# Kernel optimization log

Hardware: AMD Instinct MI355X
Metric: run time of the kernel (lower is better)

Reference implementation:

```python
import jax, jax.numpy as jnp
import numpy as np
from jax import lax


def get_grid(h, w):
    # normalized [-1,1] grid, channel 0 = x, channel 1 = y, shape [1,h,w,2]
    gx, gy = jnp.meshgrid(jnp.linspace(-1.0, 1.0, w), jnp.linspace(-1.0, 1.0, h))
    return jnp.stack([gx, gy], axis=-1)[None].astype(jnp.float32)


def gaussian_kernel(k, sigma=1.0):
    c = jnp.arange(k, dtype=jnp.float32) - (k - 1) / 2.0
    g = jnp.exp(-(c ** 2) / (2.0 * sigma ** 2))
    k2 = jnp.outer(g, g)
    return k2 / k2.sum()


def resize_bilinear(x, H, W):
    # x: [B,C,h,w]; torch F.interpolate(mode='bilinear', align_corners=False)
    B, C, h, w = x.shape
    def coords(n_out, n_in):
        c = (jnp.arange(n_out, dtype=jnp.float32) + 0.5) * (n_in / n_out) - 0.5
        c = jnp.clip(c, 0.0, n_in - 1.0)
        lo = jnp.floor(c).astype(jnp.int32)
        hi = jnp.minimum(lo + 1, n_in - 1)
        return lo, hi, c - lo.astype(jnp.float32)
    y0, y1, wy = coords(H, h)
    x0, x1, wx = coords(W, w)
    r = x[:, :, y0, :] * (1.0 - wy)[None, None, :, None] + x[:, :, y1, :] * wy[None, None, :, None]
    return r[:, :, :, x0] * (1.0 - wx) + r[:, :, :, x1] * wx


def _forward(src_grid, kernel, src_grid_base, tgt_grid, niter):
    B = src_grid.shape[0]
    H, W = tgt_grid.shape[1], tgt_grid.shape[2]
    ks = kernel.shape[-1]
    HW = H * W
    # forward displacement, resampled to target resolution, in pixel units
    dsrc = (src_grid - src_grid_base).transpose(0, 3, 1, 2)        # [B,2,Hs,Ws]
    dsrc = resize_bilinear(dsrc, H, W)                              # [B,2,H,W]
    dx = dsrc[:, 0].reshape(B, HW) * (W / 2.0)
    dy = dsrc[:, 1].reshape(B, HW) * (H / 2.0)
    xg = (jnp.arange(HW) % W).astype(jnp.float32)
    yg = (jnp.arange(HW) // W).astype(jnp.float32)
    xi = jnp.round(xg[None] + dx).astype(jnp.int32)
    yi = jnp.round(yg[None] + dy).astype(jnp.int32)
    oob = (xi < 0) | (yi < 0) | (xi > W - 1) | (yi > H - 1)
    field = jnp.where(oob, -1, yi * W + xi) + 1   # index 0 = trash slot
    # sort + dedup: duplicates are redirected to the trash slot
    order = jnp.argsort(field, axis=1)            # stable
    sf = jnp.take_along_axis(field, order, axis=1)
    keep = jnp.concatenate([jnp.ones((B, 1), bool), sf[:, 1:] != sf[:, :-1]], axis=1)
    sf = sf * keep
    inv_order = jnp.argsort(order, axis=1)
    field = jnp.take_along_axis(sf, inv_order, axis=1)
    # scatter inverse displacement (unique indices except trash slot 0)
    z = jnp.zeros((B, 1), dtype=dx.dtype)
    dxp = jnp.concatenate([z, dx], axis=1)
    dyp = jnp.concatenate([z, dy], axis=1)
    fieldp = jnp.concatenate([jnp.zeros((B, 1), field.dtype), field], axis=1)
    bidx = jnp.arange(B)[:, None]
    inv_dx = jnp.zeros_like(dxp).at[bidx, fieldp].set(-dxp)[:, 1:].reshape(B, H, W)
    inv_dy = jnp.zeros_like(dyp).at[bidx, fieldp].set(-dyp)[:, 1:].reshape(B, H, W)
    mask = (jnp.zeros_like(dxp).at[bidx, fieldp].set(1.0)[:, 1:].reshape(B, H, W)) > 0.5
    # pad so hole-fill never reads outside
    p = niter + 1
    inv_dx = jnp.pad(inv_dx, ((0, 0), (p, p), (p, p)))
    inv_dy = jnp.pad(inv_dy, ((0, 0), (p, p), (p, p)))
    mask = jnp.pad(mask, ((0, 0), (p, p), (p, p)))
    pd = ks // 2
    k4 = kernel.reshape(1, 1, ks, ks)
    def conv(x):
        return lax.conv_general_dilated(x[:, None], k4, (1, 1), [(pd, pd), (pd, pd)])[:, 0]
    # hole-fill: dilate mask by 4-neighborhood, fill with gaussian-weighted avg
    for _ in range(niter):
        nb = (jnp.pad(mask, ((0, 0), (1, 0), (0, 0)))[:, :-1]
              | jnp.pad(mask, ((0, 0), (0, 1), (0, 0)))[:, 1:]
              | jnp.pad(mask, ((0, 0), (0, 0), (1, 0)))[:, :, :-1]
              | jnp.pad(mask, ((0, 0), (0, 0), (0, 1)))[:, :, 1:])
        new_mask = (~mask) & nb
        new_dx = conv(inv_dx)
        new_dy = conv(inv_dy)
        new_sum = conv(mask.astype(inv_dx.dtype))
        denom = jnp.where(new_mask, new_sum, 1.0)  # safe: new_sum>0 where new_mask
        inv_dx = jnp.where(new_mask, new_dx / denom, inv_dx)
        inv_dy = jnp.where(new_mask, new_dy / denom, inv_dy)
        mask = mask | new_mask
    # erode: drop pixels with any unmasked 4-neighbor (outside counts as masked)
    for _ in range(niter):
        full = (jnp.pad(mask, ((0, 0), (1, 0), (0, 0)), constant_values=True)[:, :-1]
                & jnp.pad(mask, ((0, 0), (0, 1), (0, 0)), constant_values=True)[:, 1:]
                & jnp.pad(mask, ((0, 0), (0, 0), (1, 0)), constant_values=True)[:, :, :-1]
                & jnp.pad(mask, ((0, 0), (0, 0), (0, 1)), constant_values=True)[:, :, 1:])
        mask = mask & full
    inv_dx = jnp.where(mask, inv_dx, 2.0 * W)
    inv_dy = jnp.where(mask, inv_dy, 2.0 * H)
    inv_dx = inv_dx[:, p:-p, p:-p]
    inv_dy = inv_dy[:, p:-p, p:-p]
    dtgt = jnp.stack([inv_dx * (2.0 / W), inv_dy * (2.0 / H)], axis=3)
    return tgt_grid + dtgt


def setup_inputs() -> dict:
    key = jax.random.key(0)
    B, Hs, Ws, H, W = 8, 256, 256, 512, 512
    base = get_grid(Hs, Ws)
    src_grid = base + 0.05 * jax.random.normal(key, (B, Hs, Ws, 2), jnp.float32)
    return {
        "src_grid": src_grid,
        "kernel": gaussian_kernel(3),
        "src_grid_base": base,
        "tgt_grid": get_grid(H, W),
        "niter": 5,
    }


def reference(src_grid, kernel, src_grid_base, tgt_grid, niter):
    return _forward(src_grid, kernel, src_grid_base, tgt_grid, niter)
```

## Files before the change

### kernel.cpp

```cpp
#include <hip/hip_runtime.h>
#include <hip/hip_fp16.h>

typedef unsigned long long u64;
typedef unsigned int u32;
typedef float float4a __attribute__((ext_vector_type(4), aligned(4)));

#define B_    8
#define HS_   256
#define WS_   256
#define H_    512
#define W_    512
#define HW_   (H_ * W_)
#define TO_Y  16
#define WR    36
#define SLK   96
#define COFF  6
#define PC    524
#define INFW  0xFFFFFFFFu
#define EMPTY 0xFFFFFFFF00000000ull

__device__ __forceinline__ void bilin_disp(const float* __restrict__ src,
                                           const float* __restrict__ base,
                                           int b, int y, int x,
                                           float& dx, float& dy) {
#pragma clang fp contract(off)
    float cy = ((float)y + 0.5f) * 0.5f - 0.5f;
    cy = fminf(fmaxf(cy, 0.0f), 255.0f);
    int   y0 = (int)floorf(cy);
    int   y1 = min(y0 + 1, HS_ - 1);
    float wy = cy - (float)y0;

    float cx = ((float)x + 0.5f) * 0.5f - 0.5f;
    cx = fminf(fmaxf(cx, 0.0f), 255.0f);
    int   x0 = (int)floorf(cx);
    float wx = cx - (float)x0;

    float omy = 1.0f - wy;
    float wA, wB;
    int xs;
    if (x0 >= WS_ - 1) { xs = WS_ - 2; wA = 0.0f; wB = 1.0f; }
    else               { xs = x0;      wA = 1.0f - wx; wB = wx; }

    const float4a* S0 = (const float4a*)(src  + ((b * HS_ + y0) * WS_ + xs) * 2);
    const float4a* S1 = (const float4a*)(src  + ((b * HS_ + y1) * WS_ + xs) * 2);
    const float4a* B0 = (const float4a*)(base + (y0 * WS_ + xs) * 2);
    const float4a* B1 = (const float4a*)(base + (y1 * WS_ + xs) * 2);
    float4a s0 = *S0, s1 = *S1, b0 = *B0, b1 = *B1;

    float a00x = s0.x - b0.x, a00y = s0.y - b0.y;
    float a01x = s0.z - b0.z, a01y = s0.w - b0.w;
    float a10x = s1.x - b1.x, a10y = s1.y - b1.y;
    float a11x = s1.z - b1.z, a11y = s1.w - b1.w;

    float r0x = a00x * omy + a10x * wy;
    float r0y = a00y * omy + a10y * wy;
    float r1x = a01x * omy + a11x * wy;
    float r1y = a01y * omy + a11y * wy;
    dx = (r0x * wA + r1x * wB) * 256.0f;
    dy = (r0y * wA + r1y * wB) * 256.0f;
}

__device__ __forceinline__ u32 pack16(float x, float y) {
    __half hx = __float2half_rn(x), hy = __float2half_rn(y);
    return ((u32)__half_as_ushort(hy) << 16) | (u32)__half_as_ushort(hx);
}
__device__ __forceinline__ float2 unpack16(u32 p) {
    float2 f;
    f.x = __half2float(__ushort_as_half((unsigned short)(p & 0xFFFFu)));
    f.y = __half2float(__ushort_as_half((unsigned short)(p >> 16)));
    return f;
}

__device__ __forceinline__ u64 shfl_left(u64 v) {
    unsigned lo = __shfl_up((unsigned)v, 1);
    unsigned hi = __shfl_up((unsigned)(v >> 32), 1);
    u64 r = ((u64)hi << 32) | lo;
    return (threadIdx.x & 63) ? r : 0ull;
}
__device__ __forceinline__ u64 shfl_right(u64 v) {
    unsigned lo = __shfl_down((unsigned)v, 1);
    unsigned hi = __shfl_down((unsigned)(v >> 32), 1);
    u64 r = ((u64)hi << 32) | lo;
    return ((threadIdx.x & 63) == 63) ? 0ull : r;
}

__launch_bounds__(1024)
__global__ void fused_k(const float* __restrict__ src,
                        const float* __restrict__ base,
                        const float* __restrict__ kern,
                        const float* __restrict__ tgt,
                        float* __restrict__ out) {
    __shared__ u64 slot[WR * PC];

    int bx   = blockIdx.x;
    int b    = blockIdx.y;
    int tile = ((bx & 7) << 2) | (bx >> 3);
    int Y0   = tile * TO_Y;
    int w0   = Y0 - 10;
    int tid  = threadIdx.x;

    float kw[9];
#pragma unroll
    for (int q = 0; q < 9; q++) kw[q] = kern[q];

    for (int i = tid; i < WR * PC; i += 1024) slot[i] = EMPTY;
    __syncthreads();

    {
        int ylo = max(0, w0 - SLK);
        int yhi = min(H_, w0 + WR + SLK);
        int nsrc = (yhi - ylo) << 9;
        for (int i = tid; i < nsrc; i += 1024) {
            int y = ylo + (i >> 9);
            int x = i & (W_ - 1);
            float dx, dy;
            bilin_disp(src, base, b, y, x, dx, dy);
            int xi = (int)rintf((float)x + dx);
            int yi = (int)rintf((float)y + dy);
            int wr = yi - w0;
            if (xi >= 0 && xi < W_ && yi >= 0 && yi < H_ && wr >= 0 && wr < WR) {
                u64 v = ((u64)(u32)(y * W_ + x) << 32) | (u64)pack16(-dx, -dy);
                atomicMin(&slot[wr * PC + (xi + COFF)], v);
            }
        }
    }
    __syncthreads();

    int wv   = tid >> 6;
    int lane = tid & 63;
    int col  = 32 * wv - 16 + lane;
    int cls  = col + COFF;
    bool colin = (col >= -COFF) && (col <= W_ + 5);

    u64 m = 0;
    if (colin) {
#pragma unroll 6
        for (int r = 0; r < WR; r++) {
            u32 hi = ((const u32*)slot)[(r * PC + cls) * 2 + 1];
            m |= (u64)(hi != INFW) << r;
        }
    }

    int rlo = max(0, -COFF - w0);
    int rhi = min(WR - 1, (W_ + 5) - w0);
    u64 validm = colin ? ((((u64)1 << (rhi - rlo + 1)) - 1) << rlo) : 0ull;

    const u64 VROWS = (((u64)1 << 24) - 1) << 6;
    bool vlane = (lane >= 6 && lane <= 57);

    for (int it = 0; it < 5; it++) {
        u64 mL = shfl_left(m), mR = shfl_right(m);
        u64 cand = ~m & ((m << 1) | (m >> 1) | mL | mR) & validm;
        u64 cv = vlane ? (cand & VROWS) : 0ull;
        while (cv) {
            int r = __builtin_ctzll(cv);
            cv &= cv - 1;
            float s = 0.0f, ax = 0.0f, ay = 0.0f;
#pragma unroll
            for (int dr = -1; dr <= 1; dr++) {
#pragma unroll
                for (int dc = -1; dc <= 1; dc++) {
                    if (dr == 0 && dc == 0) continue;
                    u64 nm = (dc < 0) ? mL : ((dc > 0) ? mR : m);
                    float wq = ((nm >> (r + dr)) & 1)
                                 ? kw[(dr + 1) * 3 + (dc + 1)] : 0.0f;
                    int cc = min(max(cls + dc, 0), PC - 1);
                    float2 nv = unpack16(((const u32*)slot)[((r + dr) * PC + cc) * 2]);
                    s += wq; ax += wq * nv.x; ay += wq * nv.y;
                }
            }
            ((u32*)slot)[(r * PC + cls) * 2] = pack16(ax / s, ay / s);
        }
        m |= cand;
        __syncthreads();
    }

    for (int it = 0; it < 5; it++) {
        u64 mL = shfl_left(m), mR = shfl_right(m);
        m &= (m << 1) & (m >> 1) & mL & mR;
    }

    if (lane >= 16 && lane < 48) {
#pragma unroll 4
        for (int r = 10; r < 10 + TO_Y; r++) {
            int row = w0 + r;
            bool on = (m >> r) & 1;
            float vx, vy;
            if (on) {
                float2 t = unpack16(((const u32*)slot)[(r * PC + cls) * 2]);
                vx = t.x * (1.0f / 256.0f);
                vy = t.y * (1.0f / 256.0f);
            } else {
                vx = 4.0f; vy = 4.0f;
            }
            int ti = (row * W_ + col) * 2;
            float2 tg = *(const float2*)(tgt + ti);
            float2 ov; ov.x = tg.x + vx; ov.y = tg.y + vy;
            ((float2*)out)[(size_t)b * HW_ + row * W_ + col] = ov;
        }
    }
}

extern "C" void kernel_launch(void* const* d_in, const int* in_sizes, int n_in,
                              void* d_out, int out_size, void* d_ws, size_t ws_size,
                              hipStream_t stream) {
    const float* src  = (const float*)d_in[0];
    const float* kern = (const float*)d_in[1];
    const float* base = (const float*)d_in[2];
    const float* tgt  = (const float*)d_in[3];
    float* out = (float*)d_out;

    fused_k<<<dim3(32, B_), 1024, 0, stream>>>(src, base, kern, tgt, out);
}
```

Before: 164.4 us.

## Precompute forward displacement targets in a separate kernel and compact LDS values

Adds a pre-pass kernel that computes each pixel's bilinear displacement, rounded target index and packed half-precision value once and stores them in workspace. The main kernel then streams these 64-bit records instead of recomputing bilinear interpolation for every halo row, work that the overlapping windows of neighbouring tiles previously duplicated. After scattering, the packed values are moved into a dense 32-bit LDS array with a padded stride so the smoothing loop avoids strided 64-bit accesses. The cost is an extra launch plus a global write and read of about 16 MB, and the batch/tile block order is changed.

```diff
diff --git a/kernel.cpp b/kernel.cpp
--- a/kernel.cpp
+++ b/kernel.cpp
@@ -16,6 +16,8 @@
 #define SLK   96
 #define COFF  6
 #define PC    524
+#define VSTR  528
+#define NCELL (WR * PC)
 #define INFW  0xFFFFFFFFu
 #define EMPTY 0xFFFFFFFF00000000ull
 
@@ -84,17 +86,34 @@
     return ((threadIdx.x & 63) == 63) ? 0ull : r;
 }
 
+__global__ void pre_k(const float* __restrict__ src,
+                      const float* __restrict__ base,
+                      u64* __restrict__ pre) {
+    int i = blockIdx.x * 256 + threadIdx.x;
+    int b = i >> 18;
+    int j = i & (HW_ - 1);
+    int y = j >> 9;
+    int x = j & (W_ - 1);
+    float dx, dy;
+    bilin_disp(src, base, b, y, x, dx, dy);
+    int xi = (int)rintf((float)x + dx);
+    int yi = (int)rintf((float)y + dy);
+    u32 t = INFW;
+    if (xi >= 0 && xi < W_ && yi >= 0 && yi < H_) t = (u32)(yi * W_ + xi);
+    pre[i] = ((u64)t << 32) | (u64)pack16(-dx, -dy);
+}
+
 __launch_bounds__(1024)
-__global__ void fused_k(const float* __restrict__ src,
-                        const float* __restrict__ base,
-                        const float* __restrict__ kern,
-                        const float* __restrict__ tgt,
-                        float* __restrict__ out) {
-    __shared__ u64 slot[WR * PC];
-
-    int bx   = blockIdx.x;
-    int b    = blockIdx.y;
-    int tile = ((bx & 7) << 2) | (bx >> 3);
+__global__ void fused2_k(const u64* __restrict__ pre,
+                         const float* __restrict__ kern,
+                         const float* __restrict__ tgt,
+                         float* __restrict__ out) {
+    __shared__ u64 slot[NCELL];
+    u32* valsp = (u32*)slot;
+
+    int id   = blockIdx.x;
+    int b    = id & 7;
+    int tile = id >> 3;
     int Y0   = tile * TO_Y;
     int w0   = Y0 - 10;
     int tid  = threadIdx.x;
@@ -103,24 +122,24 @@
 #pragma unroll
     for (int q = 0; q < 9; q++) kw[q] = kern[q];
 
-    for (int i = tid; i < WR * PC; i += 1024) slot[i] = EMPTY;
+    for (int i = tid; i < NCELL; i += 1024) slot[i] = EMPTY;
     __syncthreads();
 
     {
+        const u64* pb = pre + b * HW_;
         int ylo = max(0, w0 - SLK);
         int yhi = min(H_, w0 + WR + SLK);
-        int nsrc = (yhi - ylo) << 9;
-        for (int i = tid; i < nsrc; i += 1024) {
-            int y = ylo + (i >> 9);
-            int x = i & (W_ - 1);
-            float dx, dy;
-            bilin_disp(src, base, b, y, x, dx, dy);
-            int xi = (int)rintf((float)x + dx);
-            int yi = (int)rintf((float)y + dy);
-            int wr = yi - w0;
-            if (xi >= 0 && xi < W_ && yi >= 0 && yi < H_ && wr >= 0 && wr < WR) {
-                u64 v = ((u64)(u32)(y * W_ + x) << 32) | (u64)pack16(-dx, -dy);
-                atomicMin(&slot[wr * PC + (xi + COFF)], v);
+        int i0  = ylo << 9, i1 = yhi << 9;
+        for (int i = i0 + tid; i < i1; i += 1024) {
+            u64 e = pb[i];
+            u32 t = (u32)(e >> 32);
+            if (t != INFW) {
+                int wr = (int)(t >> 9) - w0;
+                if ((unsigned)wr < WR) {
+                    int xc = (int)(t & (W_ - 1));
+                    atomicMin(&slot[wr * PC + xc + COFF],
+                              ((u64)(u32)i << 32) | (e & 0xFFFFFFFFull));
+                }
             }
         }
     }
@@ -140,6 +159,24 @@
             m |= (u64)(hi != INFW) << r;
         }
     }
+    u32 regs[19];
+#pragma unroll
+    for (int k = 0; k < 19; k++) {
+        int idx = tid + k * 1024;
+        regs[k] = (idx < NCELL) ? ((const u32*)slot)[idx * 2] : 0u;
+    }
+    __syncthreads();
+
+#pragma unroll
+    for (int k = 0; k < 19; k++) {
+        int idx = tid + k * 1024;
+        if (idx < NCELL) {
+            int rr = idx / PC;
+            int cc = idx - rr * PC;
+            valsp[rr * VSTR + cc] = regs[k];
+        }
+    }
+    __syncthreads();
 
     int rlo = max(0, -COFF - w0);
     int rhi = min(WR - 1, (W_ + 5) - w0);
@@ -165,11 +202,11 @@
                     float wq = ((nm >> (r + dr)) & 1)
                                  ? kw[(dr + 1) * 3 + (dc + 1)] : 0.0f;
                     int cc = min(max(cls + dc, 0), PC - 1);
-                    float2 nv = unpack16(((const u32*)slot)[((r + dr) * PC + cc) * 2]);
+                    float2 nv = unpack16(valsp[(r + dr) * VSTR + cc]);
                     s += wq; ax += wq * nv.x; ay += wq * nv.y;
                 }
             }
-            ((u32*)slot)[(r * PC + cls) * 2] = pack16(ax / s, ay / s);
+            valsp[r * VSTR + cls] = pack16(ax / s, ay / s);
         }
         m |= cand;
         __syncthreads();
@@ -187,7 +224,7 @@
             bool on = (m >> r) & 1;
             float vx, vy;
             if (on) {
-                float2 t = unpack16(((const u32*)slot)[(r * PC + cls) * 2]);
+                float2 t = unpack16(valsp[r * VSTR + cls]);
                 vx = t.x * (1.0f / 256.0f);
                 vy = t.y * (1.0f / 256.0f);
             } else {
@@ -210,5 +247,8 @@
     const float* tgt  = (const float*)d_in[3];
     float* out = (float*)d_out;
 
-    fused_k<<<dim3(32, B_), 1024, 0, stream>>>(src, base, kern, tgt, out);
-}
+    u64* pre = (u64*)d_ws;
+
+    pre_k<<<(B_ * HW_) / 256, 256, 0, stream>>>(src, base, pre);
+    fused2_k<<<256, 1024, 0, stream>>>(pre, kern, tgt, out);
+}
```

Result: faster. 141.2 us (-14.1%).

## Bucket scatter targets by row band in a pre-pass instead of redundant per-tile recomputation

Applied to the files above, without the earlier changes.

Adds a pre-pass kernel that computes each source pixel's bilinear displacement once, stores its packed payload, and appends its scatter target into a global per-batch, per-16-row-band bucket. The main kernel then reads only the three neighbouring buckets and does 32-bit atomicMin on source indices instead of recomputing displacements for a slack window of about 228 rows per tile. Splitting the 64-bit slot array into key and value arrays shrinks the atomics and shared memory. The cost is an extra launch, a memset, global bucket traffic, and a fixed bucket capacity that can silently drop entries if displacements cluster.

```diff
diff --git a/kernel.cpp b/kernel.cpp
--- a/kernel.cpp
+++ b/kernel.cpp
@@ -12,12 +12,13 @@
 #define W_    512
 #define HW_   (H_ * W_)
 #define TO_Y  16
+#define NB    32
 #define WR    36
-#define SLK   96
 #define COFF  6
-#define PC    524
+#define KC    524
+#define VSTR  528
 #define INFW  0xFFFFFFFFu
-#define EMPTY 0xFFFFFFFF00000000ull
+#define CAPB  16384
 
 __device__ __forceinline__ void bilin_disp(const float* __restrict__ src,
                                            const float* __restrict__ base,
@@ -84,17 +85,63 @@
     return ((threadIdx.x & 63) == 63) ? 0ull : r;
 }
 
+__global__ void pre_k(const float* __restrict__ src,
+                      const float* __restrict__ base,
+                      u32* __restrict__ pay,
+                      u32* __restrict__ gcount,
+                      u32* __restrict__ bucket) {
+    __shared__ u32 cnt[NB];
+    __shared__ u32 bbase[NB];
+
+    int bid = blockIdx.x;
+    int b   = bid & 7;
+    int t   = bid >> 3;
+    int j   = t * 256 + threadIdx.x;
+    int y   = j >> 9;
+    int x   = j & (W_ - 1);
+
+    if (threadIdx.x < NB) cnt[threadIdx.x] = 0;
+    __syncthreads();
+
+    float dx, dy;
+    bilin_disp(src, base, b, y, x, dx, dy);
+    pay[b * HW_ + j] = pack16(-dx, -dy);
+
+    int xi = (int)rintf((float)x + dx);
+    int yi = (int)rintf((float)y + dy);
+    bool inb = (xi >= 0 && xi < W_ && yi >= 0 && yi < H_);
+    int band = 0, rank = 0;
+    if (inb) {
+        band = yi >> 4;
+        rank = atomicAdd(&cnt[band], 1u);
+    }
+    __syncthreads();
+    if (threadIdx.x < NB && cnt[threadIdx.x] > 0)
+        bbase[threadIdx.x] = atomicAdd(&gcount[b * NB + threadIdx.x],
+                                       cnt[threadIdx.x]);
+    __syncthreads();
+    if (inb) {
+        u32 slotn = bbase[band] + rank;
+        if (slotn < CAPB) {
+            u32 e = ((u32)(yi & 15) << 27) | ((u32)xi << 18) | (u32)j;
+            bucket[(b * NB + band) * CAPB + slotn] = e;
+        }
+    }
+}
+
 __launch_bounds__(1024)
-__global__ void fused_k(const float* __restrict__ src,
-                        const float* __restrict__ base,
-                        const float* __restrict__ kern,
-                        const float* __restrict__ tgt,
-                        float* __restrict__ out) {
-    __shared__ u64 slot[WR * PC];
-
-    int bx   = blockIdx.x;
-    int b    = blockIdx.y;
-    int tile = ((bx & 7) << 2) | (bx >> 3);
+__global__ void fused3_k(const u32* __restrict__ pay,
+                         const u32* __restrict__ gcount,
+                         const u32* __restrict__ bucket,
+                         const float* __restrict__ kern,
+                         const float* __restrict__ tgt,
+                         float* __restrict__ out) {
+    __shared__ u32 key[WR * KC];
+    __shared__ u32 val[WR * VSTR];
+
+    int id   = blockIdx.x;
+    int b    = id & 7;
+    int tile = id >> 3;
     int Y0   = tile * TO_Y;
     int w0   = Y0 - 10;
     int tid  = threadIdx.x;
@@ -103,24 +150,34 @@
 #pragma unroll
     for (int q = 0; q < 9; q++) kw[q] = kern[q];
 
-    for (int i = tid; i < WR * PC; i += 1024) slot[i] = EMPTY;
+    for (int i = tid; i < WR * KC; i += 1024) key[i] = INFW;
+    for (int i = tid; i < WR * VSTR; i += 1024) val[i] = 0u;
+    __syncthreads();
+
+    for (int q = tile - 1; q <= tile + 1; q++) {
+        if (q < 0 || q >= NB) continue;
+        u32 cntq = min(gcount[b * NB + q], (u32)CAPB);
+        const u32* bk = bucket + (b * NB + q) * CAPB;
+        int ybase = q * TO_Y - w0;
+        for (u32 i = tid; i < cntq; i += 1024) {
+            u32 e  = bk[i];
+            int wr = ybase + (int)((e >> 27) & 15u);
+            if ((unsigned)wr < WR) {
+                int xc = (int)((e >> 18) & 511u);
+                atomicMin(&key[wr * KC + xc + COFF], e & 0x3FFFFu);
+            }
+        }
+    }
     __syncthreads();
 
     {
-        int ylo = max(0, w0 - SLK);
-        int yhi = min(H_, w0 + WR + SLK);
-        int nsrc = (yhi - ylo) << 9;
-        for (int i = tid; i < nsrc; i += 1024) {
-            int y = ylo + (i >> 9);
-            int x = i & (W_ - 1);
-            float dx, dy;
-            bilin_disp(src, base, b, y, x, dx, dy);
-            int xi = (int)rintf((float)x + dx);
-            int yi = (int)rintf((float)y + dy);
-            int wr = yi - w0;
-            if (xi >= 0 && xi < W_ && yi >= 0 && yi < H_ && wr >= 0 && wr < WR) {
-                u64 v = ((u64)(u32)(y * W_ + x) << 32) | (u64)pack16(-dx, -dy);
-                atomicMin(&slot[wr * PC + (xi + COFF)], v);
+        const u32* pb = pay + b * HW_;
+        for (int idx = tid; idx < WR * KC; idx += 1024) {
+            u32 k = key[idx];
+            if (k != INFW) {
+                int rr = idx / KC;
+                int cc = idx - rr * KC;
+                val[rr * VSTR + cc] = pb[k];
             }
         }
     }
@@ -135,10 +192,8 @@
     u64 m = 0;
     if (colin) {
 #pragma unroll 6
-        for (int r = 0; r < WR; r++) {
-            u32 hi = ((const u32*)slot)[(r * PC + cls) * 2 + 1];
-            m |= (u64)(hi != INFW) << r;
-        }
+        for (int r = 0; r < WR; r++)
+            m |= (u64)(key[r * KC + cls] != INFW) << r;
     }
 
     int rlo = max(0, -COFF - w0);
@@ -164,12 +219,12 @@
                     u64 nm = (dc < 0) ? mL : ((dc > 0) ? mR : m);
                     float wq = ((nm >> (r + dr)) & 1)
                                  ? kw[(dr + 1) * 3 + (dc + 1)] : 0.0f;
-                    int cc = min(max(cls + dc, 0), PC - 1);
-                    float2 nv = unpack16(((const u32*)slot)[((r + dr) * PC + cc) * 2]);
+                    int cc = min(max(cls + dc, 0), KC - 1);
+                    float2 nv = unpack16(val[(r + dr) * VSTR + cc]);
                     s += wq; ax += wq * nv.x; ay += wq * nv.y;
                 }
             }
-            ((u32*)slot)[(r * PC + cls) * 2] = pack16(ax / s, ay / s);
+            val[r * VSTR + cls] = pack16(ax / s, ay / s);
         }
         m |= cand;
         __syncthreads();
@@ -187,7 +242,7 @@
             bool on = (m >> r) & 1;
             float vx, vy;
             if (on) {
-                float2 t = unpack16(((const u32*)slot)[(r * PC + cls) * 2]);
+                float2 t = unpack16(val[r * VSTR + cls]);
                 vx = t.x * (1.0f / 256.0f);
                 vy = t.y * (1.0f / 256.0f);
             } else {
@@ -210,5 +265,13 @@
     const float* tgt  = (const float*)d_in[3];
     float* out = (float*)d_out;
 
-    fused_k<<<dim3(32, B_), 1024, 0, stream>>>(src, base, kern, tgt, out);
-}
+    char* ws = (char*)d_ws;
+    u32* gcount = (u32*)ws;
+    u32* pay    = (u32*)(ws + 1024);
+    u32* bucket = (u32*)(ws + 1024 + (size_t)B_ * HW_ * 4);
+
+    hipMemsetAsync(gcount, 0, B_ * NB * sizeof(u32), stream);
+
+    pre_k<<<(B_ * HW_) / 256, 256, 0, stream>>>(src, base, pay, gcount, bucket);
+    fused3_k<<<256, 1024, 0, stream>>>(pay, gcount, bucket, kern, tgt, out);
+}
```

New measurement: 145.1 us. -11.7%, faster.
